# Kernel tuning notes

Hardware: AMD Instinct MI355X
Metric: run time of the kernel (lower is better)

Reference implementation:

```python
import jax, jax.numpy as jnp
import numpy as np

N = 50000      # nodes
DEG = 16       # avg random degree (self-loops added on top)
IN = 256       # in_dim
HID = 32       # num_hidden per head
H = 4          # heads for hidden layers
C = 64         # num_classes (output layer has 1 head of size C)
STEPS = 10     # label_prop_steps
SLOPE = 0.2    # negative_slope


def _glorot(k, shape):
    fan = shape[0] + int(np.prod(shape[1:]))
    return jax.random.normal(k, shape, jnp.float32) * np.sqrt(2.0 / fan)


def setup_inputs() -> dict:
    key = jax.random.key(0)
    ks = jax.random.split(key, 14)
    E0 = N * DEG
    loop = jnp.arange(N, dtype=jnp.int32)
    src = jnp.concatenate([jax.random.randint(ks[0], (E0,), 0, N, jnp.int32), loop])
    dst = jnp.concatenate([jax.random.randint(ks[1], (E0,), 0, N, jnp.int32), loop])
    feat = jax.random.normal(ks[2], (N, IN), jnp.float32)
    return {
        "feat": feat, "src": src, "dst": dst,
        # layer 0: in=256 -> [4 heads, 32]
        "W0": _glorot(ks[3], (IN, H, HID)), "al0": _glorot(ks[4], (H, HID)), "ar0": _glorot(ks[5], (H, HID)),
        # layer 1: in=128 -> [4 heads, 32]
        "W1": _glorot(ks[6], (H * HID, H, HID)), "al1": _glorot(ks[7], (H, HID)), "ar1": _glorot(ks[8], (H, HID)),
        # output layer: in=128 -> [1 head, 64]
        "W2": _glorot(ks[9], (H * HID, 1, C)), "al2": _glorot(ks[10], (1, C)), "ar2": _glorot(ks[11], (1, C)),
        # weighted-pooling layer (num_classes -> num_classes, no activation)
        "Wp": _glorot(ks[12], (C, C)), "bp": jnp.zeros((C,), jnp.float32),
    }


def gat_layer(x, src, dst, W, al, ar):
    """GAT conv: returns (out [N,H,D], alpha [E,H])."""
    n = x.shape[0]
    h = jnp.einsum('ni,ihd->nhd', x, W)                    # [N,H,D]
    el = jnp.sum(h * al, axis=-1)                          # [N,H]
    er = jnp.sum(h * ar, axis=-1)                          # [N,H]
    e = el[src] + er[dst]                                  # [E,H]
    e = jnp.where(e > 0, e, SLOPE * e)                     # LeakyReLU
    m = jax.ops.segment_max(e, dst, num_segments=n)        # edge softmax over incoming edges
    p = jnp.exp(e - m[dst])
    s = jax.ops.segment_sum(p, dst, num_segments=n)
    alpha = p / (s[dst] + 1e-9)                            # [E,H]
    out = jax.ops.segment_sum(h[src] * alpha[:, :, None], dst, num_segments=n)
    return out, alpha


def reference(feat, src, dst, W0, al0, ar0, W1, al1, ar1, W2, al2, ar2, Wp, bp):
    # GAT trunk: hidden layers flatten heads + ELU, output layer means heads.
    h, a0 = gat_layer(feat, src, dst, W0, al0, ar0)
    h = jax.nn.elu(h).reshape(N, H * HID)
    h, a1 = gat_layer(h, src, dst, W1, al1, ar1)
    h = jax.nn.elu(h).reshape(N, H * HID)
    out, a2 = gat_layer(h, src, dst, W2, al2, ar2)
    logits = out.mean(axis=1)                              # [N,C]

    # mean attention over heads per layer, then over layers; detached in original
    w = jax.lax.stop_gradient(
        (a0.mean(axis=1) + a1.mean(axis=1) + a2.mean(axis=1)) / 3.0)  # [E]

    # iterative label propagation via weighted pooling + linear (num_classes->num_classes)
    pseudo = jax.nn.softmax(logits, axis=1)
    for _ in range(STEPS):
        agg = jax.ops.segment_sum(w[:, None] * pseudo[src], dst, num_segments=N)  # [N,C]
        logits = agg @ Wp + bp
        pseudo = jax.nn.softmax(logits, axis=1)
    return jnp.log(pseudo)
```

## Files before the change

kernel.cpp:

```cpp
#include <hip/hip_runtime.h>
#include <math.h>

typedef _Float16 half_t;
typedef __attribute__((ext_vector_type(2))) _Float16 half2t;
typedef __attribute__((ext_vector_type(8))) _Float16 half8;
typedef __attribute__((ext_vector_type(4))) float f32x4;

__device__ __forceinline__ half2t u2h2(unsigned u){ half2t h; __builtin_memcpy(&h, &u, 4); return h; }
__device__ __forceinline__ unsigned h22u(half2t h){ unsigned u; __builtin_memcpy(&u, &h, 4); return u; }
__device__ __forceinline__ unsigned packh2(float a, float b){
  half2t h; h[0] = (_Float16)a; h[1] = (_Float16)b; return h22u(h);
}

__device__ __forceinline__ float wsumf(float v){
#pragma unroll
  for (int off = 1; off < 64; off <<= 1) v += __shfl_xor(v, off, 64);
  return v;
}

__global__ void k_zerob(int* __restrict__ a, int n){
  int i = blockIdx.x * blockDim.x + threadIdx.x;
  if (i < n) a[i] = 0;
}

__global__ __launch_bounds__(256) void kb_hist(
    const int* __restrict__ dst, int* __restrict__ bsum, int E, int NB)
{
  __shared__ int cnt[512];
  int t = threadIdx.x;
  int e00 = blockIdx.x * 2048;
  for (int i = t; i < NB; i += 256) cnt[i] = 0;
  __syncthreads();
#pragma unroll
  for (int k = 0; k < 8; k++){
    int e = e00 + 256 * k + t;
    if (e < E) atomicAdd(&cnt[dst[e] >> 7], 1);
  }
  __syncthreads();
  for (int i = t; i < NB; i += 256){
    int c = cnt[i];
    if (c) atomicAdd(&bsum[i], c);
  }
}

__global__ __launch_bounds__(512) void kb_scan(
    const int* __restrict__ bsum, int* __restrict__ bb, int* __restrict__ gcur,
    int E, int NB)
{
  __shared__ int sh[512];
  int t = threadIdx.x;
  int v = (t < NB) ? bsum[t] : 0;
  sh[t] = v; __syncthreads();
  for (int s = 1; s < 512; s <<= 1){
    int u = (t >= s) ? sh[t - s] : 0;
    __syncthreads();
    sh[t] += u;
    __syncthreads();
  }
  if (t < NB){
    int ex = sh[t] - v;
    bb[t] = ex; gcur[t] = ex;
  }
  if (t == 0) bb[NB] = E;
}

__global__ __launch_bounds__(256) void kb_scat(
    const int* __restrict__ src, const int* __restrict__ dst,
    int* __restrict__ gcur, int2* __restrict__ ebuf, int E, int NB)
{
  __shared__ int cnt[512], base[512];
  int t = threadIdx.x;
  int e00 = blockIdx.x * 2048;
  for (int i = t; i < NB; i += 256) cnt[i] = 0;
  __syncthreads();
  int bk[8], sv[8], dv[8];
#pragma unroll
  for (int k = 0; k < 8; k++){
    int e = e00 + 256 * k + t;
    if (e < E){
      dv[k] = dst[e]; sv[k] = src[e];
      bk[k] = dv[k] >> 7;
      atomicAdd(&cnt[bk[k]], 1);
    } else bk[k] = -1;
  }
  __syncthreads();
  for (int i = t; i < NB; i += 256){
    int c = cnt[i];
    base[i] = c ? atomicAdd(&gcur[i], c) : 0;
    cnt[i] = 0;
  }
  __syncthreads();
#pragma unroll
  for (int k = 0; k < 8; k++){
    if (bk[k] >= 0){
      int pos = base[bk[k]] + atomicAdd(&cnt[bk[k]], 1);
      ebuf[pos] = make_int2(sv[k], dv[k]);
    }
  }
}

__global__ __launch_bounds__(256) void kb_sort(
    const int2* __restrict__ ebuf, const int* __restrict__ bb,
    int* __restrict__ ptre, int* __restrict__ srcs, int N, int E)
{
  __shared__ int cnt[128], off[128];
  int b = blockIdx.x, t = threadIdx.x;
  int e0 = bb[b], e1 = bb[b + 1];
  int nn0 = b << 7;
  if (t < 128) cnt[t] = 0;
  __syncthreads();
  for (int e = e0 + t; e < e1; e += 256)
    atomicAdd(&cnt[ebuf[e].y & 127], 1);
  __syncthreads();
  if (t < 128) off[t] = cnt[t];
  __syncthreads();
  for (int s = 1; s < 128; s <<= 1){
    int v = (t < 128 && t >= s) ? off[t - s] : 0;
    __syncthreads();
    if (t < 128) off[t] += v;
    __syncthreads();
  }
  if (t < 128){
    int ex = off[t] - cnt[t];
    off[t] = ex;
    int node = nn0 + t;
    if (node < N) ptre[node] = e0 + ex;
    cnt[t] = 0;
  }
  if (b == (int)gridDim.x - 1 && t == 0) ptre[N] = E;
  __syncthreads();
  for (int e = e0 + t; e < e1; e += 256){
    int2 ed = ebuf[e];
    int lo = ed.y & 127;
    int pos = atomicAdd(&cnt[lo], 1);
    srcs[e0 + off[lo] + pos] = ed.x;
  }
}

__global__ void k_cvtw(const float* __restrict__ W0, const float* __restrict__ W1,
                       const float* __restrict__ W2, const float* __restrict__ Wp,
                       half_t* __restrict__ T0, half_t* __restrict__ T1,
                       half_t* __restrict__ T2, half_t* __restrict__ Tp){
  int i = blockIdx.x * 256 + threadIdx.x;
  const float* src; half_t* dst; int NN, KK, idx;
  if (i < 32768){ src = W0; dst = T0; NN = 128; KK = 256; idx = i; }
  else if (i < 49152){ src = W1; dst = T1; NN = 128; KK = 128; idx = i - 32768; }
  else if (i < 57344){ src = W2; dst = T2; NN = 64; KK = 128; idx = i - 49152; }
  else { src = Wp; dst = Tp; NN = 64; KK = 64; idx = i - 57344; }
  int nn = idx / KK, kk = idx - nn * KK;
  dst[idx] = (_Float16)src[(size_t)kk * NN + nn];
}

template<int NC, int NH, bool XF32>
__global__ __launch_bounds__(256) void k_gemm_m(
    const void* __restrict__ Xv, const half_t* __restrict__ Wt,
    const float* __restrict__ al, const float* __restrict__ ar,
    half_t* __restrict__ Yh, float* __restrict__ el, float* __restrict__ er,
    int n, int KD)
{
  constexpr int CT = NC / 16;
  __shared__ __align__(16) half_t xs[64 * 72];
  __shared__ __align__(16) half_t ws[NC * 72];
  int tid = threadIdx.x;
  int w = tid >> 6, lane = tid & 63;
  int m = lane & 15, q = lane >> 4;
  int n0 = blockIdx.x * 64;
  f32x4 acc[CT];
#pragma unroll
  for (int ct = 0; ct < CT; ct++) acc[ct] = (f32x4){0.f, 0.f, 0.f, 0.f};

  for (int kc = 0; kc < KD; kc += 64){
    if (XF32){
      const float* X = (const float*)Xv;
#pragma unroll
      for (int s = tid; s < 512; s += 256){
        int r = s >> 3, off = (s & 7) * 8;
        int gr = min(n0 + r, n - 1);
        const float4* g = (const float4*)(X + (size_t)gr * KD + kc + off);
        float4 v0 = g[0], v1 = g[1];
        uint4 pk = make_uint4(packh2(v0.x, v0.y), packh2(v0.z, v0.w),
                              packh2(v1.x, v1.y), packh2(v1.z, v1.w));
        *(uint4*)&xs[r * 72 + off] = pk;
      }
    } else {
      const half_t* X = (const half_t*)Xv;
#pragma unroll
      for (int s = tid; s < 512; s += 256){
        int r = s >> 3, off = (s & 7) * 8;
        int gr = min(n0 + r, n - 1);
        *(uint4*)&xs[r * 72 + off] = *(const uint4*)(X + (size_t)gr * KD + kc + off);
      }
    }
#pragma unroll
    for (int s = tid; s < NC * 8; s += 256){
      int r = s >> 3, off = (s & 7) * 8;
      *(uint4*)&ws[r * 72 + off] = *(const uint4*)(Wt + (size_t)r * KD + kc + off);
    }
    __syncthreads();
    half8 a0 = *(const half8*)&xs[(16 * w + m) * 72 + q * 8];
    half8 a1 = *(const half8*)&xs[(16 * w + m) * 72 + 32 + q * 8];
#pragma unroll
    for (int ct = 0; ct < CT; ct++){
      half8 b0 = *(const half8*)&ws[(16 * ct + m) * 72 + q * 8];
      half8 b1 = *(const half8*)&ws[(16 * ct + m) * 72 + 32 + q * 8];
      acc[ct] = __builtin_amdgcn_mfma_f32_16x16x32_f16(a0, b0, acc[ct], 0, 0, 0);
      acc[ct] = __builtin_amdgcn_mfma_f32_16x16x32_f16(a1, b1, acc[ct], 0, 0, 0);
    }
    __syncthreads();
  }

#pragma unroll
  for (int j = 0; j < 4; j++){
    int gr = n0 + 16 * w + q * 4 + j;
    if (gr < n){
#pragma unroll
      for (int ct = 0; ct < CT; ct++)
        Yh[(size_t)gr * NC + 16 * ct + m] = (_Float16)acc[ct][j];
    }
  }
  float alv[CT], arv[CT];
#pragma unroll
  for (int ct = 0; ct < CT; ct++){ alv[ct] = al[16 * ct + m]; arv[ct] = ar[16 * ct + m]; }
#pragma unroll
  for (int j = 0; j < 4; j++){
    int gr = n0 + 16 * w + q * 4 + j;
    float ev[NH], rv[NH];
    if (NH == 4){
#pragma unroll
      for (int hh = 0; hh < 4; hh++){
        ev[hh] = acc[2 * hh][j] * alv[2 * hh] + acc[2 * hh + 1][j] * alv[2 * hh + 1];
        rv[hh] = acc[2 * hh][j] * arv[2 * hh] + acc[2 * hh + 1][j] * arv[2 * hh + 1];
      }
    } else {
      ev[0] = 0.f; rv[0] = 0.f;
#pragma unroll
      for (int ct = 0; ct < CT; ct++){
        ev[0] += acc[ct][j] * alv[ct];
        rv[0] += acc[ct][j] * arv[ct];
      }
    }
#pragma unroll
    for (int off = 1; off < 16; off <<= 1){
#pragma unroll
      for (int hh = 0; hh < NH; hh++){
        ev[hh] += __shfl_xor(ev[hh], off, 64);
        rv[hh] += __shfl_xor(rv[hh], off, 64);
      }
    }
    if (m == 0 && gr < n){
#pragma unroll
      for (int hh = 0; hh < NH; hh++){
        el[(size_t)gr * NH + hh] = ev[hh];
        er[(size_t)gr * NH + hh] = rv[hh];
      }
    }
  }
}

template<int HNUM, int MDIM, int EPI>
__global__ __launch_bounds__(256) void k_edge(
    const int* __restrict__ ptre, const int* __restrict__ srcs,
    const char* __restrict__ hb, const float* __restrict__ el,
    const float* __restrict__ er, half_t* __restrict__ outx,
    unsigned char* __restrict__ outu, float* __restrict__ wE,
    int2* __restrict__ epk, int init_w, int n)
{
  constexpr int LL = MDIM / 8;
  constexpr int EP = 64 / LL;
  constexpr int RB = MDIM * 2;
  int node = blockIdx.x * 4 + (threadIdx.x >> 6);
  if (node >= n) return;
  int lane = threadIdx.x & 63;
  int base = ptre[node], deg = ptre[node + 1] - base;

  float erv[HNUM];
  if (HNUM == 4){
    float4 t = *reinterpret_cast<const float4*>(er + node * 4);
    erv[0] = t.x; erv[1] = t.y; erv[2] = t.z; erv[3] = t.w;
  } else erv[0] = er[node];

  int l = lane % LL, g = lane / LL;
  int hidx = l >> 2;
  int bo = 16 * l;
  half2t acc2[4];
#pragma unroll
  for (int k = 0; k < 4; k++) acc2[k] = (half2t){(_Float16)0.f, (_Float16)0.f};

  float inv[HNUM];
  if (deg > 64){
    float sm[HNUM];
#pragma unroll
    for (int h = 0; h < HNUM; h++) sm[h] = 0.f;
    for (int i = lane; i < deg; i += 64){
      int s = srcs[base + i];
      float e[HNUM];
      if (HNUM == 4){
        float4 t = *reinterpret_cast<const float4*>(el + s * 4);
        e[0] = t.x; e[1] = t.y; e[2] = t.z; e[3] = t.w;
      } else e[0] = el[s];
#pragma unroll
      for (int h = 0; h < HNUM; h++){
        float v = e[h] + erv[h];
        v = v > 0.f ? v : 0.2f * v;
        sm[h] += __expf(v);
      }
    }
#pragma unroll
    for (int h = 0; h < HNUM; h++) inv[h] = 1.f / (wsumf(sm[h]) + 1e-9f);
  }

  for (int c0 = 0; c0 < deg; c0 += 64){
    int cnt = min(64, deg - c0);
    int soff = 0; unsigned pa = 0, pb2 = 0;
    float pv[HNUM];
    int s = 0;
    if (lane < cnt){
      s = srcs[base + c0 + lane];
      float e[HNUM];
      if (HNUM == 4){
        float4 t = *reinterpret_cast<const float4*>(el + s * 4);
        e[0] = t.x; e[1] = t.y; e[2] = t.z; e[3] = t.w;
      } else e[0] = el[s];
#pragma unroll
      for (int h = 0; h < HNUM; h++){
        float v = e[h] + erv[h];
        v = v > 0.f ? v : 0.2f * v;
        pv[h] = __expf(v);
      }
    } else {
#pragma unroll
      for (int h = 0; h < HNUM; h++) pv[h] = 0.f;
    }
    if (deg <= 64){
#pragma unroll
      for (int h = 0; h < HNUM; h++) inv[h] = 1.f / (wsumf(pv[h]) + 1e-9f);
    }
    if (lane < cnt){
      float a[HNUM], wsum = 0.f;
#pragma unroll
      for (int h = 0; h < HNUM; h++){ a[h] = pv[h] * inv[h]; wsum += a[h]; }
      if (HNUM == 4){ pa = packh2(a[0], a[1]); pb2 = packh2(a[2], a[3]); }
      else pa = packh2(a[0], a[0]);
      wsum *= (1.f / (3.f * HNUM));
      int eidx = base + c0 + lane;
      if (EPI == 1){
        float wtot = (wE[eidx] + wsum) * (1.f / 255.f);
        epk[eidx] = make_int2(s * 64, __float_as_int(wtot));
      } else {
        wE[eidx] = init_w ? wsum : (wE[eidx] + wsum);
      }
      soff = s * RB;
    }
    for (int j0 = 0; j0 < cnt; j0 += EP){
      int j = j0 + g;
      int so = __shfl(soff, j, 64);
      unsigned paj = (unsigned)__shfl((int)pa, j, 64);
      unsigned pbj = 0;
      if (HNUM == 4) pbj = (unsigned)__shfl((int)pb2, j, 64);
      if (j < cnt){
        unsigned a2u;
        if (HNUM == 4){
          unsigned sel = (hidx < 2) ? paj : pbj;
          unsigned hb16 = (hidx & 1) ? (sel >> 16) : (sel & 0xffffu);
          a2u = hb16 | (hb16 << 16);
        } else a2u = paj;
        half2t a2 = u2h2(a2u);
        uint4 v = *(const uint4*)(hb + (unsigned)so + bo);
        acc2[0] += a2 * u2h2(v.x);
        acc2[1] += a2 * u2h2(v.y);
        acc2[2] += a2 * u2h2(v.z);
        acc2[3] += a2 * u2h2(v.w);
      }
    }
  }

#pragma unroll
  for (int off = LL; off < 64; off <<= 1)
#pragma unroll
    for (int k = 0; k < 4; k++)
      acc2[k] += u2h2((unsigned)__shfl_xor((int)h22u(acc2[k]), off, 64));

  float o[8];
#pragma unroll
  for (int k = 0; k < 4; k++){
    o[2 * k] = (float)acc2[k][0];
    o[2 * k + 1] = (float)acc2[k][1];
  }
  if (EPI == 0){
    if (g == 0){
#pragma unroll
      for (int d = 0; d < 8; d++) o[d] = o[d] > 0.f ? o[d] : expm1f(o[d]);
      uint4 pk = make_uint4(packh2(o[0], o[1]), packh2(o[2], o[3]),
                            packh2(o[4], o[5]), packh2(o[6], o[7]));
      reinterpret_cast<uint4*>(outx + (size_t)node * MDIM)[l] = pk;
    }
  } else {
    float m8 = o[0];
#pragma unroll
    for (int d = 1; d < 8; d++) m8 = fmaxf(m8, o[d]);
#pragma unroll
    for (int off = 1; off < 8; off <<= 1) m8 = fmaxf(m8, __shfl_xor(m8, off, 64));
    float p[8], s8 = 0.f;
#pragma unroll
    for (int d = 0; d < 8; d++){ p[d] = __expf(o[d] - m8); s8 += p[d]; }
#pragma unroll
    for (int off = 1; off < 8; off <<= 1) s8 += __shfl_xor(s8, off, 64);
    float is = 255.f / s8;
    if (g == 0){
      unsigned b0 = 0, b1 = 0;
#pragma unroll
      for (int d = 0; d < 4; d++) b0 |= ((unsigned)(int)(p[d] * is + 0.5f)) << (8 * d);
#pragma unroll
      for (int d = 0; d < 4; d++) b1 |= ((unsigned)(int)(p[4 + d] * is + 0.5f)) << (8 * d);
      *reinterpret_cast<uint2*>(outu + (size_t)node * 64 + 8 * l) = make_uint2(b0, b1);
    }
  }
}

template<int FINAL>
__global__ __launch_bounds__(512) void k_lpu(
    const int* __restrict__ ptre, const int2* __restrict__ epk,
    const unsigned char* __restrict__ pb, const half_t* __restrict__ Tp,
    const float* __restrict__ bp, unsigned char* __restrict__ outu,
    float* __restrict__ outf, int n)
{
  __shared__ __align__(16) half_t xs[64 * 72];
  __shared__ __align__(16) half_t ws[64 * 72];
  __shared__ float bsh[64];
  int tid = threadIdx.x;
  int w = tid >> 6, lane = tid & 63;
  int n0 = blockIdx.x * 64;
  {
    int r = tid >> 3, off = (tid & 7) * 8;
    *(uint4*)&ws[r * 72 + off] = *(const uint4*)(Tp + r * 64 + off);
  }
  if (tid < 64) bsh[tid] = bp[tid];

  int grp = tid >> 3;
  int l8 = tid & 7;
  int st = l8 >> 2, li = l8 & 3;
  int bo = 16 * li;
  int node = n0 + grp;
  float acc[16];
#pragma unroll
  for (int c = 0; c < 16; c++) acc[c] = 0.f;

  auto accum = [&](uint4 v, float wv){
#pragma unroll
    for (int b = 0; b < 4; b++){
      unsigned u = (&v.x)[b];
      acc[4 * b + 0] += wv * (float)(u & 0xffu);
      acc[4 * b + 1] += wv * (float)((u >> 8) & 0xffu);
      acc[4 * b + 2] += wv * (float)((u >> 16) & 0xffu);
      acc[4 * b + 3] += wv * (float)((u >> 24) & 0xffu);
    }
  };

  if (node < n){
    int base = ptre[node], endd = ptre[node + 1];
    for (int j0 = base + 4 * st; j0 < endd; j0 += 8){
      int2 ee[4]; float wv[4];
#pragma unroll
      for (int k = 0; k < 4; k++){
        int j = j0 + k;
        ee[k] = epk[min(j, endd - 1)];
        wv[k] = (j < endd) ? __int_as_float(ee[k].y) : 0.f;
      }
      uint4 vv[4];
#pragma unroll
      for (int k = 0; k < 4; k++)
        vv[k] = *(const uint4*)(pb + (unsigned)ee[k].x + bo);
#pragma unroll
      for (int k = 0; k < 4; k++) accum(vv[k], wv[k]);
    }
  }
#pragma unroll
  for (int c = 0; c < 16; c++) acc[c] += __shfl_xor(acc[c], 4, 64);
  if (st == 0){
    half2t hp[8];
#pragma unroll
    for (int c = 0; c < 8; c++){
      hp[c][0] = (_Float16)acc[2 * c]; hp[c][1] = (_Float16)acc[2 * c + 1];
    }
    *(uint4*)&xs[grp * 72 + 16 * li]     = *(uint4*)&hp[0];
    *(uint4*)&xs[grp * 72 + 16 * li + 8] = *(uint4*)&hp[4];
  }
  __syncthreads();
  if (w >= 4) return;

  int m = lane & 15, q = lane >> 4;
  f32x4 macc[4];
#pragma unroll
  for (int ct = 0; ct < 4; ct++) macc[ct] = (f32x4){0.f, 0.f, 0.f, 0.f};
  half8 a0 = *(const half8*)&xs[(16 * w + m) * 72 + q * 8];
  half8 a1 = *(const half8*)&xs[(16 * w + m) * 72 + 32 + q * 8];
#pragma unroll
  for (int ct = 0; ct < 4; ct++){
    half8 b0 = *(const half8*)&ws[(16 * ct + m) * 72 + q * 8];
    half8 b1 = *(const half8*)&ws[(16 * ct + m) * 72 + 32 + q * 8];
    macc[ct] = __builtin_amdgcn_mfma_f32_16x16x32_f16(a0, b0, macc[ct], 0, 0, 0);
    macc[ct] = __builtin_amdgcn_mfma_f32_16x16x32_f16(a1, b1, macc[ct], 0, 0, 0);
  }

#pragma unroll
  for (int j = 0; j < 4; j++){
    int gr = n0 + 16 * w + q * 4 + j;
    float v[4]; float mx = -INFINITY;
#pragma unroll
    for (int ct = 0; ct < 4; ct++){
      v[ct] = macc[ct][j] + bsh[16 * ct + m];
      mx = fmaxf(mx, v[ct]);
    }
#pragma unroll
    for (int off = 1; off < 16; off <<= 1) mx = fmaxf(mx, __shfl_xor(mx, off, 64));
    float p[4], s = 0.f;
#pragma unroll
    for (int ct = 0; ct < 4; ct++){ p[ct] = __expf(v[ct] - mx); s += p[ct]; }
#pragma unroll
    for (int off = 1; off < 16; off <<= 1) s += __shfl_xor(s, off, 64);
    if (gr < n){
      if (FINAL){
        float ls = __logf(s);
#pragma unroll
        for (int ct = 0; ct < 4; ct++)
          outf[(size_t)gr * 64 + 16 * ct + m] = v[ct] - mx - ls;
      } else {
        float is = 255.f / s;
#pragma unroll
        for (int ct = 0; ct < 4; ct++)
          outu[(size_t)gr * 64 + 16 * ct + m] =
              (unsigned char)(int)(p[ct] * is + 0.5f);
      }
    }
  }
}

extern "C" void kernel_launch(void* const* d_in, const int* in_sizes, int n_in,
                              void* d_out, int out_size, void* d_ws, size_t ws_size,
                              hipStream_t stream) {
  const float* feat = (const float*)d_in[0];
  const int*   src  = (const int*)d_in[1];
  const int*   dst  = (const int*)d_in[2];
  const float* W0   = (const float*)d_in[3];
  const float* al0  = (const float*)d_in[4];
  const float* ar0  = (const float*)d_in[5];
  const float* W1   = (const float*)d_in[6];
  const float* al1  = (const float*)d_in[7];
  const float* ar1  = (const float*)d_in[8];
  const float* W2   = (const float*)d_in[9];
  const float* al2  = (const float*)d_in[10];
  const float* ar2  = (const float*)d_in[11];
  const float* Wp   = (const float*)d_in[12];
  const float* bp   = (const float*)d_in[13];
  float* out = (float*)d_out;

  const int N = in_sizes[0] / 256;
  const int E = in_sizes[1];
  const int NB = (N + 127) / 128;

  char* p = (char*)d_ws;
  auto carve = [&](size_t bytes) -> void* {
    void* r = (void*)p;
    p += (bytes + 255) & ~(size_t)255;
    return r;
  };
  int*   ptr_i = (int*)carve((size_t)(N + 1) * 4);
  int*   bsum  = (int*)carve((size_t)NB * 4);
  int*   bb    = (int*)carve((size_t)(NB + 1) * 4);
  int*   gcur  = (int*)carve((size_t)NB * 4);
  int*   srcs  = (int*)carve((size_t)E * 4);
  float* wE    = (float*)carve((size_t)E * 4);
  int2*  epk   = (int2*)carve((size_t)E * 8);
  half_t* hb   = (half_t*)carve((size_t)N * 128 * 2);
  half_t* xb   = (half_t*)carve((size_t)N * 128 * 2);
  float* el    = (float*)carve((size_t)N * 4 * 4);
  float* er    = (float*)carve((size_t)N * 4 * 4);
  unsigned char* pbA = (unsigned char*)carve((size_t)N * 64);
  unsigned char* pbB = (unsigned char*)carve((size_t)N * 64);
  half_t* T0   = (half_t*)carve(32768 * 2);
  half_t* T1   = (half_t*)carve(16384 * 2);
  half_t* T2   = (half_t*)carve(8192 * 2);
  half_t* Tp   = (half_t*)carve(4096 * 2);
  int2* ebuf = epk;
  (void)ws_size; (void)n_in; (void)out_size;

  const int EB = (E + 2047) / 2048;
  k_zerob<<<(NB + 255) / 256, 256, 0, stream>>>(bsum, NB);
  kb_hist<<<EB, 256, 0, stream>>>(dst, bsum, E, NB);
  kb_scan<<<1, 512, 0, stream>>>(bsum, bb, gcur, E, NB);
  kb_scat<<<EB, 256, 0, stream>>>(src, dst, gcur, ebuf, E, NB);
  kb_sort<<<NB, 256, 0, stream>>>(ebuf, bb, ptr_i, srcs, N, E);
  k_cvtw<<<240, 256, 0, stream>>>(W0, W1, W2, Wp, T0, T1, T2, Tp);

  const int GG = (N + 63) / 64;
  const int GE = (N + 3) / 4;
  k_gemm_m<128, 4, true><<<GG, 256, 0, stream>>>(feat, T0, al0, ar0, hb, el, er, N, 256);
  k_edge<4, 128, 0><<<GE, 256, 0, stream>>>(ptr_i, srcs, (const char*)hb, el, er,
                                            xb, nullptr, wE, nullptr, 1, N);
  k_gemm_m<128, 4, false><<<GG, 256, 0, stream>>>(xb, T1, al1, ar1, hb, el, er, N, 128);
  k_edge<4, 128, 0><<<GE, 256, 0, stream>>>(ptr_i, srcs, (const char*)hb, el, er,
                                            xb, nullptr, wE, nullptr, 0, N);
  k_gemm_m<64, 1, false><<<GG, 256, 0, stream>>>(xb, T2, al2, ar2, hb, el, er, N, 128);
  k_edge<1, 64, 1><<<GE, 256, 0, stream>>>(ptr_i, srcs, (const char*)hb, el, er,
                                           nullptr, pbA, wE, epk, 0, N);

  unsigned char* cur = pbA; unsigned char* nxt = pbB;
  for (int st = 0; st < 10; st++){
    if (st == 9)
      k_lpu<1><<<GG, 512, 0, stream>>>(ptr_i, epk, cur, Tp, bp, nullptr, out, N);
    else
      k_lpu<0><<<GG, 512, 0, stream>>>(ptr_i, epk, cur, Tp, bp, nxt, nullptr, N);
    unsigned char* t = cur; cur = nxt; nxt = t;
  }
}
```

Baseline: 475.2 us.

## Fuse ten label-propagation steps into one persistent cooperative kernel with grid sync

Replaces the ten separate label-propagation kernel launches with a single cooperative persistent kernel. It loops over the steps internally, ping-pongs the uint8 pseudo-label buffers and separates steps with grid.sync, loading the pooling weights into shared memory once. The aim is to cut per-launch overhead and tail effects across the iterations. The costs are lower occupancy from 256-thread blocks sized by the occupancy query and the price of grid-wide barriers. The old per-step launch path stays as a fallback if the cooperative launch fails.

New measurement: 1.209 ms. 2.55x slower.

```diff
diff --git a/kernel.cpp b/kernel.cpp
--- a/kernel.cpp
+++ b/kernel.cpp
@@ -1,5 +1,8 @@
 #include <hip/hip_runtime.h>
+#include <hip/hip_cooperative_groups.h>
 #include <math.h>
+
+namespace cg = cooperative_groups;
 
 typedef _Float16 half_t;
 typedef __attribute__((ext_vector_type(2))) _Float16 half2t;
@@ -532,6 +535,138 @@
               (unsigned char)(int)(p[ct] * is + 0.5f);
       }
     }
+  }
+}
+
+__global__ __launch_bounds__(256) void k_lp10(
+    const int* __restrict__ ptre, const int2* __restrict__ epk,
+    unsigned char* __restrict__ pbA, unsigned char* __restrict__ pbB,
+    const half_t* __restrict__ Tp, const float* __restrict__ bp,
+    float* __restrict__ outf, int n, int ntiles)
+{
+  cg::grid_group grid = cg::this_grid();
+  __shared__ __align__(16) half_t xs[64 * 72];
+  __shared__ __align__(16) half_t ws[64 * 72];
+  __shared__ float bsh[64];
+  int tid = threadIdx.x;
+  int w = tid >> 6, lane = tid & 63;
+  for (int s = tid; s < 512; s += 256){
+    int r = s >> 3, off = (s & 7) * 8;
+    *(uint4*)&ws[r * 72 + off] = *(const uint4*)(Tp + r * 64 + off);
+  }
+  if (tid < 64) bsh[tid] = bp[tid];
+  __syncthreads();
+
+  int grp = tid >> 2, l4 = tid & 3;
+  int bo = 16 * l4;
+  int m = lane & 15, q = lane >> 4;
+
+  for (int st = 0; st < 10; st++){
+    const unsigned char* cur = (st & 1) ? pbB : pbA;
+    unsigned char* nxt = (st & 1) ? pbA : pbB;
+    for (int t = blockIdx.x; t < ntiles; t += gridDim.x){
+      int n0 = t * 64;
+      int node = n0 + grp;
+      float acc[16];
+#pragma unroll
+      for (int c = 0; c < 16; c++) acc[c] = 0.f;
+      if (node < n){
+        int j = ptre[node], endd = ptre[node + 1];
+        while (j + 4 <= endd){
+          int2 e0 = epk[j], e1 = epk[j + 1], e2 = epk[j + 2], e3 = epk[j + 3];
+          uint4 v0 = *(const uint4*)(cur + (unsigned)e0.x + bo);
+          uint4 v1 = *(const uint4*)(cur + (unsigned)e1.x + bo);
+          uint4 v2 = *(const uint4*)(cur + (unsigned)e2.x + bo);
+          uint4 v3 = *(const uint4*)(cur + (unsigned)e3.x + bo);
+          float w0 = __int_as_float(e0.y), w1 = __int_as_float(e1.y);
+          float w2 = __int_as_float(e2.y), w3 = __int_as_float(e3.y);
+#pragma unroll
+          for (int b = 0; b < 4; b++){
+            unsigned u0 = (&v0.x)[b], u1 = (&v1.x)[b], u2 = (&v2.x)[b], u3 = (&v3.x)[b];
+#pragma unroll
+            for (int c = 0; c < 4; c++){
+              int sh = 8 * c;
+              acc[4 * b + c] += w0 * (float)((u0 >> sh) & 0xffu)
+                              + w1 * (float)((u1 >> sh) & 0xffu)
+                              + w2 * (float)((u2 >> sh) & 0xffu)
+                              + w3 * (float)((u3 >> sh) & 0xffu);
+            }
+          }
+          j += 4;
+        }
+        while (j < endd){
+          int2 ep = epk[j];
+          uint4 v = *(const uint4*)(cur + (unsigned)ep.x + bo);
+          float wv = __int_as_float(ep.y);
+#pragma unroll
+          for (int b = 0; b < 4; b++){
+            unsigned u = (&v.x)[b];
+#pragma unroll
+            for (int c = 0; c < 4; c++)
+              acc[4 * b + c] += wv * (float)((u >> (8 * c)) & 0xffu);
+          }
+          j++;
+        }
+      }
+      {
+        half2t hp[8];
+#pragma unroll
+        for (int c = 0; c < 8; c++){
+          hp[c][0] = (_Float16)acc[2 * c]; hp[c][1] = (_Float16)acc[2 * c + 1];
+        }
+        *(uint4*)&xs[grp * 72 + 16 * l4]     = *(uint4*)&hp[0];
+        *(uint4*)&xs[grp * 72 + 16 * l4 + 8] = *(uint4*)&hp[4];
+      }
+      __syncthreads();
+      {
+        f32x4 macc[4];
+#pragma unroll
+        for (int ct = 0; ct < 4; ct++) macc[ct] = (f32x4){0.f, 0.f, 0.f, 0.f};
+        half8 a0 = *(const half8*)&xs[(16 * w + m) * 72 + q * 8];
+        half8 a1 = *(const half8*)&xs[(16 * w + m) * 72 + 32 + q * 8];
+#pragma unroll
+        for (int ct = 0; ct < 4; ct++){
+          half8 b0 = *(const half8*)&ws[(16 * ct + m) * 72 + q * 8];
+          half8 b1 = *(const half8*)&ws[(16 * ct + m) * 72 + 32 + q * 8];
+          macc[ct] = __builtin_amdgcn_mfma_f32_16x16x32_f16(a0, b0, macc[ct], 0, 0, 0);
+          macc[ct] = __builtin_amdgcn_mfma_f32_16x16x32_f16(a1, b1, macc[ct], 0, 0, 0);
+        }
+#pragma unroll
+        for (int j = 0; j < 4; j++){
+          int gr = n0 + 16 * w + q * 4 + j;
+          float v[4]; float mx = -INFINITY;
+#pragma unroll
+          for (int ct = 0; ct < 4; ct++){
+            v[ct] = macc[ct][j] + bsh[16 * ct + m];
+            mx = fmaxf(mx, v[ct]);
+          }
+#pragma unroll
+          for (int off = 1; off < 16; off <<= 1) mx = fmaxf(mx, __shfl_xor(mx, off, 64));
+          float p[4], s = 0.f;
+#pragma unroll
+          for (int ct = 0; ct < 4; ct++){ p[ct] = __expf(v[ct] - mx); s += p[ct]; }
+#pragma unroll
+          for (int off = 1; off < 16; off <<= 1) s += __shfl_xor(s, off, 64);
+          if (gr < n){
+            if (st == 9){
+              float ls = __logf(s);
+#pragma unroll
+              for (int ct = 0; ct < 4; ct++)
+                outf[(size_t)gr * 64 + 16 * ct + m] = v[ct] - mx - ls;
+            } else {
+              float is = 255.f / s;
+#pragma unroll
+              for (int ct = 0; ct < 4; ct++)
+                nxt[(size_t)gr * 64 + 16 * ct + m] =
+                    (unsigned char)(int)(p[ct] * is + 0.5f);
+            }
+          }
+        }
+      }
+      __syncthreads();
+    }
+    __threadfence();
+    grid.sync();
   }
 }
 
@@ -604,12 +739,27 @@
   k_edge<1, 64, 1><<<GE, 256, 0, stream>>>(ptr_i, srcs, (const char*)hb, el, er,
                                            nullptr, pbA, wE, epk, 0, N);
 
-  unsigned char* cur = pbA; unsigned char* nxt = pbB;
-  for (int st = 0; st < 10; st++){
-    if (st == 9)
-      k_lpu<1><<<GG, 512, 0, stream>>>(ptr_i, epk, cur, Tp, bp, nullptr, out, N);
-    else
-      k_lpu<0><<<GG, 512, 0, stream>>>(ptr_i, epk, cur, Tp, bp, nxt, nullptr, N);
-    unsigned char* t = cur; cur = nxt; nxt = t;
-  }
-}
+  int ntiles = GG;
+  int occ = 0;
+  hipError_t oerr = hipOccupancyMaxActiveBlocksPerMultiprocessor(
+      &occ, (const void*)k_lp10, 256, 0);
+  int grid = (oerr == hipSuccess && occ > 0) ? occ * 256 : 0;
+  if (grid > ntiles) grid = ntiles;
+  hipError_t lerr = hipErrorInvalidValue;
+  if (grid > 0){
+    void* args[] = { (void*)&ptr_i, (void*)&epk, (void*)&pbA, (void*)&pbB,
+                     (void*)&Tp, (void*)&bp, (void*)&out, (void*)&N, (void*)&ntiles };
+    lerr = hipLaunchCooperativeKernel((void*)k_lp10, dim3(grid), dim3(256),
+                                      args, 0, stream);
+  }
+  if (lerr != hipSuccess){
+    unsigned char* cur = pbA; unsigned char* nxt = pbB;
+    for (int st = 0; st < 10; st++){
+      if (st == 9)
+        k_lpu<1><<<GG, 512, 0, stream>>>(ptr_i, epk, cur, Tp, bp, nullptr, out, N);
+      else
+        k_lpu<0><<<GG, 512, 0, stream>>>(ptr_i, epk, cur, Tp, bp, nxt, nullptr, N);
+      unsigned char* t = cur; cur = nxt; nxt = t;
+    }
+  }
+}
```

## Make label-propagation kernel wave-local with shuffles instead of shared memory

Applied to the files above, without the earlier changes.

Rewrites the label-propagation step so each wavefront gathers 16 nodes with 4 lanes per node, then rearranges the fp16 aggregates into MFMA A-fragments through cross-lane shuffles. This drops the shared-memory staging, the block barrier and the idle half-block that only did gathering. The projection weights and bias are loaded directly into registers per wave. In exchange, each lane walks a node's whole edge list with 8 edges unrolled instead of splitting it over two lanes, so per-lane serial work rises and register pressure grows.

Result: slower. 522.2 us (+9.9%).

```diff
diff --git a/kernel.cpp b/kernel.cpp
--- a/kernel.cpp
+++ b/kernel.cpp
@@ -418,97 +418,97 @@
 }
 
 template<int FINAL>
-__global__ __launch_bounds__(512) void k_lpu(
+__global__ __launch_bounds__(256) void k_lpw(
     const int* __restrict__ ptre, const int2* __restrict__ epk,
     const unsigned char* __restrict__ pb, const half_t* __restrict__ Tp,
     const float* __restrict__ bp, unsigned char* __restrict__ outu,
     float* __restrict__ outf, int n)
 {
-  __shared__ __align__(16) half_t xs[64 * 72];
-  __shared__ __align__(16) half_t ws[64 * 72];
-  __shared__ float bsh[64];
   int tid = threadIdx.x;
   int w = tid >> 6, lane = tid & 63;
-  int n0 = blockIdx.x * 64;
-  {
-    int r = tid >> 3, off = (tid & 7) * 8;
-    *(uint4*)&ws[r * 72 + off] = *(const uint4*)(Tp + r * 64 + off);
-  }
-  if (tid < 64) bsh[tid] = bp[tid];
-
-  int grp = tid >> 3;
-  int l8 = tid & 7;
-  int st = l8 >> 2, li = l8 & 3;
-  int bo = 16 * li;
-  int node = n0 + grp;
+  int wbase = (blockIdx.x * 4 + w) * 16;
+  if (wbase >= n) return;
+  int mD = lane & 15, qD = lane >> 4;
+
+  half8 bf0[4], bf1[4]; float bv[4];
+#pragma unroll
+  for (int ct = 0; ct < 4; ct++){
+    bf0[ct] = *(const half8*)(Tp + (16 * ct + mD) * 64 + qD * 8);
+    bf1[ct] = *(const half8*)(Tp + (16 * ct + mD) * 64 + 32 + qD * 8);
+    bv[ct] = bp[16 * ct + mD];
+  }
+
+  int gnode = wbase + (lane >> 2);
+  int l4 = lane & 3, bo = 16 * l4;
   float acc[16];
 #pragma unroll
   for (int c = 0; c < 16; c++) acc[c] = 0.f;
-
-  auto accum = [&](uint4 v, float wv){
-#pragma unroll
-    for (int b = 0; b < 4; b++){
-      unsigned u = (&v.x)[b];
-      acc[4 * b + 0] += wv * (float)(u & 0xffu);
-      acc[4 * b + 1] += wv * (float)((u >> 8) & 0xffu);
-      acc[4 * b + 2] += wv * (float)((u >> 16) & 0xffu);
-      acc[4 * b + 3] += wv * (float)((u >> 24) & 0xffu);
-    }
-  };
-
-  if (node < n){
-    int base = ptre[node], endd = ptre[node + 1];
-    for (int j0 = base + 4 * st; j0 < endd; j0 += 8){
-      int2 ee[4]; float wv[4];
-#pragma unroll
-      for (int k = 0; k < 4; k++){
-        int j = j0 + k;
-        ee[k] = epk[min(j, endd - 1)];
-        wv[k] = (j < endd) ? __int_as_float(ee[k].y) : 0.f;
-      }
-      uint4 vv[4];
-#pragma unroll
-      for (int k = 0; k < 4; k++)
+  if (gnode < n){
+    int jb = ptre[gnode], endd = ptre[gnode + 1];
+    for (int j0 = jb; j0 < endd; j0 += 8){
+      int2 ee[8]; float wv[8];
+#pragma unroll
+      for (int k = 0; k < 8; k++){
+        int jj = j0 + k;
+        ee[k] = epk[min(jj, endd - 1)];
+        wv[k] = (jj < endd) ? __int_as_float(ee[k].y) : 0.f;
+      }
+      uint4 vv[8];
+#pragma unroll
+      for (int k = 0; k < 8; k++)
         vv[k] = *(const uint4*)(pb + (unsigned)ee[k].x + bo);
 #pragma unroll
-      for (int k = 0; k < 4; k++) accum(vv[k], wv[k]);
-    }
-  }
-#pragma unroll
-  for (int c = 0; c < 16; c++) acc[c] += __shfl_xor(acc[c], 4, 64);
-  if (st == 0){
-    half2t hp[8];
-#pragma unroll
-    for (int c = 0; c < 8; c++){
-      hp[c][0] = (_Float16)acc[2 * c]; hp[c][1] = (_Float16)acc[2 * c + 1];
-    }
-    *(uint4*)&xs[grp * 72 + 16 * li]     = *(uint4*)&hp[0];
-    *(uint4*)&xs[grp * 72 + 16 * li + 8] = *(uint4*)&hp[4];
-  }
-  __syncthreads();
-  if (w >= 4) return;
-
-  int m = lane & 15, q = lane >> 4;
+      for (int k = 0; k < 8; k++){
+        float wvk = wv[k];
+#pragma unroll
+        for (int b = 0; b < 4; b++){
+          unsigned u = (&vv[k].x)[b];
+          acc[4 * b + 0] += wvk * (float)(u & 0xffu);
+          acc[4 * b + 1] += wvk * (float)((u >> 8) & 0xffu);
+          acc[4 * b + 2] += wvk * (float)((u >> 16) & 0xffu);
+          acc[4 * b + 3] += wvk * (float)((u >> 24) & 0xffu);
+        }
+      }
+    }
+  }
+
+  unsigned d[8];
+#pragma unroll
+  for (int c = 0; c < 8; c++) d[c] = packh2(acc[2 * c], acc[2 * c + 1]);
+
+  int s0 = mD * 4 + (qD >> 1);
+  int s1 = s0 + 2;
+  int hi = qD & 1;
+  unsigned a0w[4], a1w[4];
+#pragma unroll
+  for (int j = 0; j < 4; j++){
+    unsigned lo0 = (unsigned)__shfl((int)d[j], s0, 64);
+    unsigned hi0 = (unsigned)__shfl((int)d[4 + j], s0, 64);
+    a0w[j] = hi ? hi0 : lo0;
+    unsigned lo1 = (unsigned)__shfl((int)d[j], s1, 64);
+    unsigned hi1 = (unsigned)__shfl((int)d[4 + j], s1, 64);
+    a1w[j] = hi ? hi1 : lo1;
+  }
+  half8 a0, a1;
+  __builtin_memcpy(&a0, a0w, 16);
+  __builtin_memcpy(&a1, a1w, 16);
+
   f32x4 macc[4];
 #pragma unroll
   for (int ct = 0; ct < 4; ct++) macc[ct] = (f32x4){0.f, 0.f, 0.f, 0.f};
-  half8 a0 = *(const half8*)&xs[(16 * w + m) * 72 + q * 8];
-  half8 a1 = *(const half8*)&xs[(16 * w + m) * 72 + 32 + q * 8];
 #pragma unroll
   for (int ct = 0; ct < 4; ct++){
-    half8 b0 = *(const half8*)&ws[(16 * ct + m) * 72 + q * 8];
-    half8 b1 = *(const half8*)&ws[(16 * ct + m) * 72 + 32 + q * 8];
-    macc[ct] = __builtin_amdgcn_mfma_f32_16x16x32_f16(a0, b0, macc[ct], 0, 0, 0);
-    macc[ct] = __builtin_amdgcn_mfma_f32_16x16x32_f16(a1, b1, macc[ct], 0, 0, 0);
+    macc[ct] = __builtin_amdgcn_mfma_f32_16x16x32_f16(a0, bf0[ct], macc[ct], 0, 0, 0);
+    macc[ct] = __builtin_amdgcn_mfma_f32_16x16x32_f16(a1, bf1[ct], macc[ct], 0, 0, 0);
   }
 
 #pragma unroll
   for (int j = 0; j < 4; j++){
-    int gr = n0 + 16 * w + q * 4 + j;
+    int gr = wbase + qD * 4 + j;
     float v[4]; float mx = -INFINITY;
 #pragma unroll
     for (int ct = 0; ct < 4; ct++){
-      v[ct] = macc[ct][j] + bsh[16 * ct + m];
+      v[ct] = macc[ct][j] + bv[ct];
       mx = fmaxf(mx, v[ct]);
     }
 #pragma unroll
@@ -523,12 +523,12 @@
         float ls = __logf(s);
 #pragma unroll
         for (int ct = 0; ct < 4; ct++)
-          outf[(size_t)gr * 64 + 16 * ct + m] = v[ct] - mx - ls;
+          outf[(size_t)gr * 64 + 16 * ct + mD] = v[ct] - mx - ls;
       } else {
         float is = 255.f / s;
 #pragma unroll
         for (int ct = 0; ct < 4; ct++)
-          outu[(size_t)gr * 64 + 16 * ct + m] =
+          outu[(size_t)gr * 64 + 16 * ct + mD] =
               (unsigned char)(int)(p[ct] * is + 0.5f);
       }
     }
@@ -607,9 +607,9 @@
   unsigned char* cur = pbA; unsigned char* nxt = pbB;
   for (int st = 0; st < 10; st++){
     if (st == 9)
-      k_lpu<1><<<GG, 512, 0, stream>>>(ptr_i, epk, cur, Tp, bp, nullptr, out, N);
+      k_lpw<1><<<GG, 256, 0, stream>>>(ptr_i, epk, cur, Tp, bp, nullptr, out, N);
     else
-      k_lpu<0><<<GG, 512, 0, stream>>>(ptr_i, epk, cur, Tp, bp, nxt, nullptr, N);
+      k_lpw<0><<<GG, 256, 0, stream>>>(ptr_i, epk, cur, Tp, bp, nxt, nullptr, N);
     unsigned char* t = cur; cur = nxt; nxt = t;
   }
 }
```
